# Kernel optimization log

Hardware: AMD Instinct MI355X
Metric: run time of the kernel (lower is better)

Reference implementation:

```python
import jax, jax.numpy as jnp
import numpy as np

N_NODES = 50000
N_EDGES = 800000
DIM_IN = 64
DIM_HID = 128
DIM_OUT = 64


def _linear_init(key, fan_in, fan_out):
    # torch nn.Linear default: U(-1/sqrt(fan_in), 1/sqrt(fan_in)) for W and b
    kw, kb = jax.random.split(key)
    bound = 1.0 / np.sqrt(fan_in)
    W = jax.random.uniform(kw, (fan_in, fan_out), minval=-bound, maxval=bound, dtype=jnp.float32)
    b = jax.random.uniform(kb, (fan_out,), minval=-bound, maxval=bound, dtype=jnp.float32)
    return W, b


def setup_inputs() -> dict:
    key = jax.random.key(0)
    kx, ke, k0, k1, k2 = jax.random.split(key, 5)
    x = jax.random.normal(kx, (N_NODES, DIM_IN), dtype=jnp.float32)
    edge_idx = jax.random.randint(ke, (2, N_EDGES), 0, N_NODES, dtype=jnp.int64)
    W0, b0 = _linear_init(k0, 2 * DIM_IN, DIM_HID)
    W1, b1 = _linear_init(k1, DIM_HID, DIM_HID)
    W2, b2 = _linear_init(k2, DIM_HID, DIM_OUT)
    return {"x": x, "edge_idx": edge_idx, "W0": W0, "b0": b0,
            "W1": W1, "b1": b1, "W2": W2, "b2": b2}


def reference(x, edge_idx, W0, b0, W1, b1, W2, b2):
    row, col = edge_idx[0], edge_idx[1]
    # gather + concat edge features: [E, 2*dim_in]
    h = jnp.concatenate([x[row], x[col]], axis=-1)
    h = jax.nn.softplus(h @ W0 + b0)
    h = jax.nn.softplus(h @ W1 + b1)
    h = h @ W2 + b2  # [E, dim_out]
    # scatter-add edge messages to source nodes
    return jax.ops.segment_sum(h, row, num_segments=x.shape[0])
```

## Files before the change

kernel.cpp:

```cpp
#include <hip/hip_runtime.h>
#include <math.h>

#define N_NODES 50000
#define N_EDGES 800000
#define DIM_IN 64
#define DIM_HID 128
#define DIM_OUT 64

#define EB  128
#define PAD 136

typedef __attribute__((ext_vector_type(8))) short short8;
typedef __attribute__((ext_vector_type(4))) float f32x4;

__device__ __forceinline__ unsigned short f2bf(float f) {
    unsigned u = __float_as_uint(f);
    unsigned r = (u + 0x7fffu + ((u >> 16) & 1u)) >> 16;
    return (unsigned short)r;
}

__device__ __forceinline__ float softplus_f(float v) {
    float e = __expf(-fabsf(v));
    return fmaxf(v, 0.0f) + __logf(1.0f + e);
}

__global__ void zero_out_kernel(float4* __restrict__ out, int n4) {
    int i = blockIdx.x * blockDim.x + threadIdx.x;
    if (i < n4) out[i] = make_float4(0.f, 0.f, 0.f, 0.f);
}

__global__ void prep_weights(const float* __restrict__ W0,
                             const float* __restrict__ W1,
                             const float* __restrict__ W2,
                             unsigned short* __restrict__ wt) {
    const int R = 128 * PAD;
    int i = blockIdx.x * blockDim.x + threadIdx.x;
    if (i < R) {
        int n = i / PAD, k = i - n * PAD;
        wt[i] = f2bf(k < 128 ? W0[k * DIM_HID + n] : 0.f);
    } else if (i < 2 * R) {
        int j = i - R;
        int n = j / PAD, k = j - n * PAD;
        wt[i] = f2bf(k < 128 ? W1[k * DIM_HID + n] : 0.f);
    } else if (i < 2 * R + 64 * PAD) {
        int j = i - 2 * R;
        int n = j / PAD, k = j - n * PAD;
        wt[i] = f2bf(k < 128 ? W2[k * DIM_OUT + n] : 0.f);
    }
}

__global__ __launch_bounds__(256, 2)
void edge_mlp_mfma(const float* __restrict__ x,
                   const int* __restrict__ eidx,
                   const unsigned short* __restrict__ wt,
                   const float* __restrict__ b0,
                   const float* __restrict__ b1,
                   const float* __restrict__ b2,
                   float* __restrict__ out) {
    __shared__ unsigned short Ha[EB * PAD];
    __shared__ int rowS[EB];
    __shared__ int colS[EB];

    const int tid = threadIdx.x;
    const int e0 = blockIdx.x * EB;

    if (tid < EB) {
        rowS[tid] = eidx[e0 + tid];
        colS[tid] = eidx[N_EDGES + e0 + tid];
    }
    __syncthreads();

#pragma unroll
    for (int it = 0; it < 16; ++it) {
        int f = tid + it * 256;
        int e = f >> 5;
        int c = f & 31;
        int src = (c & 16) ? colS[e] : rowS[e];
        float4 v = *(const float4*)(x + (size_t)src * DIM_IN + (c & 15) * 4);
        unsigned p0 = f2bf(v.x) | ((unsigned)f2bf(v.y) << 16);
        unsigned p1 = f2bf(v.z) | ((unsigned)f2bf(v.w) << 16);
        *(uint2*)(Ha + e * PAD + c * 4) = make_uint2(p0, p1);
    }
    __syncthreads();

    const int lane = tid & 63;
    const int w = tid >> 6;
    const int wi = w & 1;
    const int wj = w >> 1;
    const int l16 = lane & 15;
    const int q = lane >> 4;

    const unsigned short* Wt0 = wt;
    const unsigned short* Wt1 = wt + 128 * PAD;
    const unsigned short* Wt2 = wt + 256 * PAD;

#pragma unroll 1
    for (int layer = 0; layer < 2; ++layer) {
        const unsigned short* W = layer ? Wt1 : Wt0;
        const float* bias = layer ? b1 : b0;

        short8 afr[4][4];
#pragma unroll
        for (int ss = 0; ss < 4; ++ss)
#pragma unroll
            for (int kk = 0; kk < 4; ++kk)
                afr[ss][kk] = *(const short8*)(Ha + (wi * 64 + ss * 16 + l16) * PAD + kk * 32 + q * 8);
        __syncthreads();

        f32x4 acc[4][4];
#pragma unroll
        for (int ss = 0; ss < 4; ++ss)
#pragma unroll
            for (int tt = 0; tt < 4; ++tt)
                acc[ss][tt] = (f32x4){0.f, 0.f, 0.f, 0.f};

#pragma unroll
        for (int tt = 0; tt < 4; ++tt) {
            const unsigned short* Wp = W + (wj * 64 + tt * 16 + l16) * PAD + q * 8;
            short8 bfr[4];
#pragma unroll
            for (int kk = 0; kk < 4; ++kk)
                bfr[kk] = *(const short8*)(Wp + kk * 32);
#pragma unroll
            for (int ss = 0; ss < 4; ++ss)
#pragma unroll
                for (int kk = 0; kk < 4; ++kk)
                    acc[ss][tt] = __builtin_amdgcn_mfma_f32_16x16x32_bf16(
                        afr[ss][kk], bfr[kk], acc[ss][tt], 0, 0, 0);
        }

#pragma unroll
        for (int tt = 0; tt < 4; ++tt) {
            float bv = bias[wj * 64 + tt * 16 + l16];
#pragma unroll
            for (int ss = 0; ss < 4; ++ss) {
#pragma unroll
                for (int r = 0; r < 4; ++r) {
                    float vv = softplus_f(acc[ss][tt][r] + bv);
                    Ha[(wi * 64 + ss * 16 + q * 4 + r) * PAD + wj * 64 + tt * 16 + l16] = f2bf(vv);
                }
            }
        }
        __syncthreads();
    }

    {
        short8 afr[4][4];
#pragma unroll
        for (int ss = 0; ss < 4; ++ss)
#pragma unroll
            for (int kk = 0; kk < 4; ++kk)
                afr[ss][kk] = *(const short8*)(Ha + (wi * 64 + ss * 16 + l16) * PAD + kk * 32 + q * 8);

        f32x4 acc[4][2];
#pragma unroll
        for (int ss = 0; ss < 4; ++ss)
#pragma unroll
            for (int tt = 0; tt < 2; ++tt)
                acc[ss][tt] = (f32x4){0.f, 0.f, 0.f, 0.f};

#pragma unroll
        for (int tt = 0; tt < 2; ++tt) {
            const unsigned short* Wp = Wt2 + (wj * 32 + tt * 16 + l16) * PAD + q * 8;
            short8 bfr[4];
#pragma unroll
            for (int kk = 0; kk < 4; ++kk)
                bfr[kk] = *(const short8*)(Wp + kk * 32);
#pragma unroll
            for (int ss = 0; ss < 4; ++ss)
#pragma unroll
                for (int kk = 0; kk < 4; ++kk)
                    acc[ss][tt] = __builtin_amdgcn_mfma_f32_16x16x32_bf16(
                        afr[ss][kk], bfr[kk], acc[ss][tt], 0, 0, 0);
        }

        float bv0 = b2[wj * 32 + l16];
        float bv1 = b2[wj * 32 + 16 + l16];
#pragma unroll
        for (int ss = 0; ss < 4; ++ss) {
#pragma unroll
            for (int r = 0; r < 4; ++r) {
                int row = wi * 64 + ss * 16 + q * 4 + r;
                int node = rowS[row];
                float* op = out + (size_t)node * DIM_OUT + wj * 32 + l16;
                atomicAdd(op, acc[ss][0][r] + bv0);
                atomicAdd(op + 16, acc[ss][1][r] + bv1);
            }
        }
    }
}

extern "C" void kernel_launch(void* const* d_in, const int* in_sizes, int n_in,
                              void* d_out, int out_size, void* d_ws, size_t ws_size,
                              hipStream_t stream) {
    const float* x  = (const float*)d_in[0];
    const int*   ei = (const int*)d_in[1];
    const float* W0 = (const float*)d_in[2];
    const float* b0 = (const float*)d_in[3];
    const float* W1 = (const float*)d_in[4];
    const float* b1 = (const float*)d_in[5];
    const float* W2 = (const float*)d_in[6];
    const float* b2 = (const float*)d_in[7];
    float* out = (float*)d_out;
    unsigned short* wt = (unsigned short*)d_ws;

    const int n4 = (N_NODES * DIM_OUT) / 4;
    zero_out_kernel<<<(n4 + 255) / 256, 256, 0, stream>>>((float4*)out, n4);

    const int wn = 2 * 128 * PAD + 64 * PAD;
    prep_weights<<<(wn + 255) / 256, 256, 0, stream>>>(W0, W1, W2, wt);

    edge_mlp_mfma<<<N_EDGES / EB, 256, 0, stream>>>(x, ei, wt, b0, b1, b2, out);
}
```

Before: 320.0 us.

## Give each wave its own 32-edge tile and drop block-wide barriers

```diff
diff --git a/kernel.cpp b/kernel.cpp
--- a/kernel.cpp
+++ b/kernel.cpp
@@ -15,18 +15,21 @@
 
 __device__ __forceinline__ unsigned short f2bf(float f) {
     unsigned u = __float_as_uint(f);
-    unsigned r = (u + 0x7fffu + ((u >> 16) & 1u)) >> 16;
-    return (unsigned short)r;
+    return (unsigned short)((u + 0x7fffu + ((u >> 16) & 1u)) >> 16);
+}
+
+__device__ __forceinline__ short8 pack8(float4 a, float4 b) {
+    short8 f;
+    f[0] = (short)f2bf(a.x); f[1] = (short)f2bf(a.y);
+    f[2] = (short)f2bf(a.z); f[3] = (short)f2bf(a.w);
+    f[4] = (short)f2bf(b.x); f[5] = (short)f2bf(b.y);
+    f[6] = (short)f2bf(b.z); f[7] = (short)f2bf(b.w);
+    return f;
 }
 
 __device__ __forceinline__ float softplus_f(float v) {
     float e = __expf(-fabsf(v));
     return fmaxf(v, 0.0f) + __logf(1.0f + e);
-}
-
-__global__ void zero_out_kernel(float4* __restrict__ out, int n4) {
-    int i = blockIdx.x * blockDim.x + threadIdx.x;
-    if (i < n4) out[i] = make_float4(0.f, 0.f, 0.f, 0.f);
 }
 
 __global__ void prep_weights(const float* __restrict__ W0,
@@ -49,7 +52,35 @@
     }
 }
 
-__global__ __launch_bounds__(256, 2)
+template <int NT>
+__device__ __forceinline__ void mfma_layer(const short8 afr[2][4],
+                                           const unsigned short* __restrict__ W,
+                                           const float* __restrict__ bias,
+                                           f32x4 acc[2][8], int l16, int q) {
+#pragma unroll
+    for (int t = 0; t < NT; ++t) {
+        float bv = bias[t * 16 + l16];
+#pragma unroll
+        for (int m = 0; m < 2; ++m)
+            acc[m][t] = (f32x4){bv, bv, bv, bv};
+    }
+#pragma unroll
+    for (int t = 0; t < NT; ++t) {
+        const unsigned short* Wp = W + (t * 16 + l16) * PAD + q * 8;
+        short8 bfr[4];
+#pragma unroll
+        for (int kk = 0; kk < 4; ++kk)
+            bfr[kk] = *(const short8*)(Wp + kk * 32);
+#pragma unroll
+        for (int m = 0; m < 2; ++m)
+#pragma unroll
+            for (int kk = 0; kk < 4; ++kk)
+                acc[m][t] = __builtin_amdgcn_mfma_f32_16x16x32_bf16(
+                    afr[m][kk], bfr[kk], acc[m][t], 0, 0, 0);
+    }
+}
+
+__global__ __launch_bounds__(256, 3)
 void edge_mlp_mfma(const float* __restrict__ x,
                    const int* __restrict__ eidx,
                    const unsigned short* __restrict__ wt,
@@ -57,137 +88,89 @@
                    const float* __restrict__ b1,
                    const float* __restrict__ b2,
                    float* __restrict__ out) {
-    __shared__ unsigned short Ha[EB * PAD];
-    __shared__ int rowS[EB];
-    __shared__ int colS[EB];
+    __shared__ unsigned short Ha[4][32 * PAD];
 
-    const int tid = threadIdx.x;
-    const int e0 = blockIdx.x * EB;
-
-    if (tid < EB) {
-        rowS[tid] = eidx[e0 + tid];
-        colS[tid] = eidx[N_EDGES + e0 + tid];
-    }
-    __syncthreads();
-
-#pragma unroll
-    for (int it = 0; it < 16; ++it) {
-        int f = tid + it * 256;
-        int e = f >> 5;
-        int c = f & 31;
-        int src = (c & 16) ? colS[e] : rowS[e];
-        float4 v = *(const float4*)(x + (size_t)src * DIM_IN + (c & 15) * 4);
-        unsigned p0 = f2bf(v.x) | ((unsigned)f2bf(v.y) << 16);
-        unsigned p1 = f2bf(v.z) | ((unsigned)f2bf(v.w) << 16);
-        *(uint2*)(Ha + e * PAD + c * 4) = make_uint2(p0, p1);
-    }
-    __syncthreads();
-
+    const int tid  = threadIdx.x;
     const int lane = tid & 63;
-    const int w = tid >> 6;
-    const int wi = w & 1;
-    const int wj = w >> 1;
-    const int l16 = lane & 15;
-    const int q = lane >> 4;
+    const int w    = tid >> 6;
+    const int l16  = lane & 15;
+    const int q    = lane >> 4;
+    const int e0w  = blockIdx.x * EB + w * 32;
+    unsigned short* Hw = &Ha[w][0];
 
     const unsigned short* Wt0 = wt;
     const unsigned short* Wt1 = wt + 128 * PAD;
     const unsigned short* Wt2 = wt + 256 * PAD;
 
-#pragma unroll 1
-    for (int layer = 0; layer < 2; ++layer) {
-        const unsigned short* W = layer ? Wt1 : Wt0;
-        const float* bias = layer ? b1 : b0;
+    int rowI[2], colI[2];
+#pragma unroll
+    for (int m = 0; m < 2; ++m) {
+        rowI[m] = eidx[e0w + m * 16 + l16];
+        colI[m] = eidx[N_EDGES + e0w + m * 16 + l16];
+    }
 
-        short8 afr[4][4];
+    short8 afr[2][4];
 #pragma unroll
-        for (int ss = 0; ss < 4; ++ss)
+    for (int m = 0; m < 2; ++m)
 #pragma unroll
-            for (int kk = 0; kk < 4; ++kk)
-                afr[ss][kk] = *(const short8*)(Ha + (wi * 64 + ss * 16 + l16) * PAD + kk * 32 + q * 8);
-        __syncthreads();
+        for (int kk = 0; kk < 4; ++kk) {
+            int node = (kk < 2) ? rowI[m] : colI[m];
+            const float* p = x + (size_t)node * DIM_IN + (kk & 1) * 32 + q * 8;
+            float4 va = *(const float4*)p;
+            float4 vb = *(const float4*)(p + 4);
+            afr[m][kk] = pack8(va, vb);
+        }
 
-        f32x4 acc[4][4];
-#pragma unroll
-        for (int ss = 0; ss < 4; ++ss)
-#pragma unroll
-            for (int tt = 0; tt < 4; ++tt)
-                acc[ss][tt] = (f32x4){0.f, 0.f, 0.f, 0.f};
+    f32x4 acc[2][8];
+    mfma_layer<8>(afr, Wt0, b0, acc, l16, q);
 
 #pragma unroll
-        for (int tt = 0; tt < 4; ++tt) {
-            const unsigned short* Wp = W + (wj * 64 + tt * 16 + l16) * PAD + q * 8;
-            short8 bfr[4];
+    for (int m = 0; m < 2; ++m)
 #pragma unroll
-            for (int kk = 0; kk < 4; ++kk)
-                bfr[kk] = *(const short8*)(Wp + kk * 32);
+        for (int t = 0; t < 8; ++t)
 #pragma unroll
-            for (int ss = 0; ss < 4; ++ss)
-#pragma unroll
-                for (int kk = 0; kk < 4; ++kk)
-                    acc[ss][tt] = __builtin_amdgcn_mfma_f32_16x16x32_bf16(
-                        afr[ss][kk], bfr[kk], acc[ss][tt], 0, 0, 0);
-        }
+            for (int r = 0; r < 4; ++r)
+                Hw[(m * 16 + q * 4 + r) * PAD + t * 16 + l16] =
+                    f2bf(softplus_f(acc[m][t][r]));
+    asm volatile("s_waitcnt lgkmcnt(0)" ::: "memory");
 
 #pragma unroll
-        for (int tt = 0; tt < 4; ++tt) {
-            float bv = bias[wj * 64 + tt * 16 + l16];
+    for (int m = 0; m < 2; ++m)
 #pragma unroll
-            for (int ss = 0; ss < 4; ++ss) {
-#pragma unroll
-                for (int r = 0; r < 4; ++r) {
-                    float vv = softplus_f(acc[ss][tt][r] + bv);
-                    Ha[(wi * 64 + ss * 16 + q * 4 + r) * PAD + wj * 64 + tt * 16 + l16] = f2bf(vv);
-                }
-            }
-        }
-        __syncthreads();
-    }
+        for (int kk = 0; kk < 4; ++kk)
+            afr[m][kk] = *(const short8*)(Hw + (m * 16 + l16) * PAD + kk * 32 + q * 8);
 
-    {
-        short8 afr[4][4];
-#pragma unroll
-        for (int ss = 0; ss < 4; ++ss)
-#pragma unroll
-            for (int kk = 0; kk < 4; ++kk)
-                afr[ss][kk] = *(const short8*)(Ha + (wi * 64 + ss * 16 + l16) * PAD + kk * 32 + q * 8);
-
-        f32x4 acc[4][2];
-#pragma unroll
-        for (int ss = 0; ss < 4; ++ss)
-#pragma unroll
-            for (int tt = 0; tt < 2; ++tt)
-                acc[ss][tt] = (f32x4){0.f, 0.f, 0.f, 0.f};
+    mfma_layer<8>(afr, Wt1, b1, acc, l16, q);
 
 #pragma unroll
-        for (int tt = 0; tt < 2; ++tt) {
-            const unsigned short* Wp = Wt2 + (wj * 32 + tt * 16 + l16) * PAD + q * 8;
-            short8 bfr[4];
+    for (int m = 0; m < 2; ++m)
 #pragma unroll
-            for (int kk = 0; kk < 4; ++kk)
-                bfr[kk] = *(const short8*)(Wp + kk * 32);
+        for (int t = 0; t < 8; ++t)
 #pragma unroll
-            for (int ss = 0; ss < 4; ++ss)
+            for (int r = 0; r < 4; ++r)
+                Hw[(m * 16 + q * 4 + r) * PAD + t * 16 + l16] =
+                    f2bf(softplus_f(acc[m][t][r]));
+    asm volatile("s_waitcnt lgkmcnt(0)" ::: "memory");
+
 #pragma unroll
-                for (int kk = 0; kk < 4; ++kk)
-                    acc[ss][tt] = __builtin_amdgcn_mfma_f32_16x16x32_bf16(
-                        afr[ss][kk], bfr[kk], acc[ss][tt], 0, 0, 0);
+    for (int m = 0; m < 2; ++m)
+#pragma unroll
+        for (int kk = 0; kk < 4; ++kk)
+            afr[m][kk] = *(const short8*)(Hw + (m * 16 + l16) * PAD + kk * 32 + q * 8);
+
+    mfma_layer<4>(afr, Wt2, b2, acc, l16, q);
+
+#pragma unroll
+    for (int m = 0; m < 2; ++m)
+#pragma unroll
+        for (int r = 0; r < 4; ++r) {
+            int node = eidx[e0w + m * 16 + q * 4 + r];
+            float* op = out + (size_t)node * DIM_OUT + l16;
+            atomicAdd(op,      acc[m][0][r]);
+            atomicAdd(op + 16, acc[m][1][r]);
+            atomicAdd(op + 32, acc[m][2][r]);
+            atomicAdd(op + 48, acc[m][3][r]);
         }
-
-        float bv0 = b2[wj * 32 + l16];
-        float bv1 = b2[wj * 32 + 16 + l16];
-#pragma unroll
-        for (int ss = 0; ss < 4; ++ss) {
-#pragma unroll
-            for (int r = 0; r < 4; ++r) {
-                int row = wi * 64 + ss * 16 + q * 4 + r;
-                int node = rowS[row];
-                float* op = out + (size_t)node * DIM_OUT + wj * 32 + l16;
-                atomicAdd(op, acc[ss][0][r] + bv0);
-                atomicAdd(op + 16, acc[ss][1][r] + bv1);
-            }
-        }
-    }
 }
 
 extern "C" void kernel_launch(void* const* d_in, const int* in_sizes, int n_in,
@@ -204,8 +187,7 @@
     float* out = (float*)d_out;
     unsigned short* wt = (unsigned short*)d_ws;
 
-    const int n4 = (N_NODES * DIM_OUT) / 4;
-    zero_out_kernel<<<(n4 + 255) / 256, 256, 0, stream>>>((float4*)out, n4);
+    hipMemsetAsync(out, 0, (size_t)N_NODES * DIM_OUT * sizeof(float), stream);
 
     const int wn = 2 * 128 * PAD + 64 * PAD;
     prep_weights<<<(wn + 255) / 256, 256, 0, stream>>>(W0, W1, W2, wt);
```

Measured after the change: 306.8 us. -4.1%, faster.
